# Kernel optimization log

Hardware: AMD Instinct MI355X
Metric: run time of the kernel (lower is better)

## Reference

```python
import jax, jax.numpy as jnp
import numpy as np

HIDDEN = 1024
HEADS = 16
HEAD_DIM = HIDDEN // HEADS
ROPE_BASE = 10000.0


def rope_cos_sin(seq_len, head_dim, dtype=jnp.float32):
    inv_freq = 1.0 / (ROPE_BASE ** (jnp.arange(0, head_dim, 2, dtype=jnp.float32) / head_dim))
    t = jnp.arange(seq_len, dtype=jnp.float32)
    freqs = jnp.einsum('i,j->ij', t, inv_freq)          # [L, head_dim/2]
    emb = jnp.concatenate([freqs, freqs], axis=-1)       # [L, head_dim]
    return emb.astype(dtype), jnp.cos(emb).astype(dtype), jnp.sin(emb).astype(dtype)


def rotate_half(x):
    half = x.shape[-1] // 2
    return jnp.concatenate([-x[..., half:], x[..., :half]], axis=-1)


def setup_inputs() -> dict:
    key = jax.random.key(0)
    kx, kq, kk, kv, ko = jax.random.split(key, 5)
    B, L = 4, 2048
    scale = 1.0 / np.sqrt(HIDDEN)
    x = jax.random.normal(kx, (B, L, HIDDEN), dtype=jnp.float32)
    Wq = jax.random.normal(kq, (HIDDEN, HIDDEN), dtype=jnp.float32) * scale
    Wk = jax.random.normal(kk, (HIDDEN, HIDDEN), dtype=jnp.float32) * scale
    Wv = jax.random.normal(kv, (HIDDEN, HIDDEN), dtype=jnp.float32) * scale
    Wo = jax.random.normal(ko, (HIDDEN, HIDDEN), dtype=jnp.float32) * scale
    return {"x": x, "Wq": Wq, "Wk": Wk, "Wv": Wv, "Wo": Wo}


def reference(x, Wq, Wk, Wv, Wo):
    B, L, D = x.shape
    H, Hd = HEADS, HEAD_DIM
    # projections (nn.Linear: y = x @ W.T; weights here stored already as [out,in])
    q = (x @ Wq.T).reshape(B, L, H, Hd).transpose(0, 2, 1, 3)  # [B,H,L,Hd]
    k = (x @ Wk.T).reshape(B, L, H, Hd).transpose(0, 2, 1, 3)
    v = (x @ Wv.T).reshape(B, L, H, Hd).transpose(0, 2, 1, 3)
    _, cos, sin = rope_cos_sin(L, Hd, x.dtype)                  # [L, Hd]
    cos = cos[None, None, :, :]
    sin = sin[None, None, :, :]
    q = q * cos + rotate_half(q) * sin
    k = k * cos + rotate_half(k) * sin
    scores = jnp.einsum('bhqd,bhkd->bhqk', q, k) / np.sqrt(Hd)  # [B,H,L,L]
    attn = jax.nn.softmax(scores, axis=-1)
    out = jnp.einsum('bhqk,bhkd->bhqd', attn, v)                # [B,H,L,Hd]
    out = out.transpose(0, 2, 1, 3).reshape(B, L, D)
    return out @ Wo.T
```

## Files before the change

kernel.cpp:

```cpp
#include <hip/hip_runtime.h>
#include <math.h>

#define BB 4
#define LL 2048
#define DD 1024
#define HH 16
#define HD 64
#define BL (BB*LL)

typedef __attribute__((ext_vector_type(8))) short bf16x8;
typedef __attribute__((ext_vector_type(4))) short bf16x4;
typedef __attribute__((ext_vector_type(4))) float f32x4;

__device__ inline short f2bf(float f) {
    union { float f; unsigned u; } v; v.f = f;
    unsigned r = v.u + 0x7fffu + ((v.u >> 16) & 1u);
    return (short)(r >> 16);
}

__device__ inline unsigned pk_bf16(float a, float b) {
    union { float f; unsigned u; } x, y; x.f = a; y.f = b;
    return (x.u >> 16) | (y.u & 0xffff0000u);
}

__device__ inline float exp2x(float x) {
#if __has_builtin(__builtin_amdgcn_exp2f)
    return __builtin_amdgcn_exp2f(x);
#else
    return exp2f(x);
#endif
}

__device__ inline f32x4 mfma16x16x16_bf16(bf16x4 a, bf16x4 b, f32x4 c) {
#if __has_builtin(__builtin_amdgcn_mfma_f32_16x16x16bf16_1k)
    return __builtin_amdgcn_mfma_f32_16x16x16bf16_1k(a, b, c, 0, 0, 0);
#elif __has_builtin(__builtin_amdgcn_mfma_f32_16x16x16_bf16)
    return __builtin_amdgcn_mfma_f32_16x16x16_bf16(a, b, c, 0, 0, 0);
#else
    f32x4 d;
    asm volatile("v_mfma_f32_16x16x16_bf16 %0, %1, %2, %3"
                 : "=v"(d) : "v"(a), "v"(b), "v"(c));
    return d;
#endif
}

__device__ inline void gload_lds16(const void* g, void* l) {
    __builtin_amdgcn_global_load_lds(
        (const __attribute__((address_space(1))) unsigned int*)g,
        (__attribute__((address_space(3))) unsigned int*)l, 16, 0, 0);
}

__global__ __launch_bounds__(256) void cast_kernel(
    const float* __restrict__ in, short* __restrict__ out, int n)
{
    int i = (blockIdx.x * 256 + threadIdx.x) * 8;
    float4 a = *(const float4*)(in + i);
    float4 b = *(const float4*)(in + i + 4);
    bf16x8 o;
    o[0]=f2bf(a.x); o[1]=f2bf(a.y); o[2]=f2bf(a.z); o[3]=f2bf(a.w);
    o[4]=f2bf(b.x); o[5]=f2bf(b.y); o[6]=f2bf(b.z); o[7]=f2bf(b.w);
    *(bf16x8*)(out + i) = o;
}

__global__ __launch_bounds__(256) void cast4_kernel(
    const float* __restrict__ w0, const float* __restrict__ w1,
    const float* __restrict__ w2, const float* __restrict__ w3,
    short* __restrict__ out)
{
    const int nw_blocks = (DD*DD) / 2048;
    int sel = blockIdx.x / nw_blocks;
    int blk = blockIdx.x % nw_blocks;
    const float* in = (sel == 0) ? w0 : (sel == 1) ? w1 : (sel == 2) ? w2 : w3;
    int i = (blk * 256 + threadIdx.x) * 8;
    float4 a = *(const float4*)(in + i);
    float4 b = *(const float4*)(in + i + 4);
    bf16x8 o;
    o[0]=f2bf(a.x); o[1]=f2bf(a.y); o[2]=f2bf(a.z); o[3]=f2bf(a.w);
    o[4]=f2bf(b.x); o[5]=f2bf(b.y); o[6]=f2bf(b.z); o[7]=f2bf(b.w);
    *(bf16x8*)(out + (size_t)sel * DD * DD + i) = o;
}

__global__ __launch_bounds__(256) void rope_tab_kernel(float2* __restrict__ tab)
{
    int idx = blockIdx.x * 256 + threadIdx.x;
    int lq = idx >> 5, f = idx & 31;
    float inv = __expf((float)f * (-9.210340371976184f / 32.0f));
    float s, c;
    sincosf((float)lq * inv, &s, &c);
    tab[idx] = make_float2(c, s);
}

__device__ inline void gemm_bt_128(const short* __restrict__ A,
                                   const short* __restrict__ B,
                                   short* Ash, short* Bsh,
                                   int i0, int n0, f32x4 (&acc)[4][4])
{
    const int t  = threadIdx.x;
    const int w  = t >> 6;
    const int l  = t & 63;
    const int g  = (t >> 4) & 3;
    const int ln = t & 15;
    const int rh = (w >> 1) * 64;
    const int ch = (w & 1) * 64;
    const int srow = w * 8 + (l >> 3);
    const int skol = (l & 7) * 8;

    for (int k0 = 0; k0 < DD; k0 += 64) {
        __syncthreads();
        const short* ga = A + (size_t)(i0 + srow) * DD + k0 + skol;
        const short* gb = B + (size_t)(n0 + srow) * DD + k0 + skol;
        short* la = Ash + w * 512;
        short* lb = Bsh + w * 512;
        #pragma unroll
        for (int j = 0; j < 4; ++j) {
            gload_lds16(ga + j * 32 * DD, la + j * 2048);
            gload_lds16(gb + j * 32 * DD, lb + j * 2048);
        }
        __syncthreads();

        #pragma unroll
        for (int kk = 0; kk < 2; ++kk) {
            bf16x8 af[4], bfr[4];
            #pragma unroll
            for (int mi = 0; mi < 4; ++mi)
                af[mi] = *(const bf16x8*)(Ash + (rh + mi*16 + ln)*64 + kk*32 + 8*g);
            #pragma unroll
            for (int nj = 0; nj < 4; ++nj)
                bfr[nj] = *(const bf16x8*)(Bsh + (ch + nj*16 + ln)*64 + kk*32 + 8*g);
            #pragma unroll
            for (int mi = 0; mi < 4; ++mi)
                #pragma unroll
                for (int nj = 0; nj < 4; ++nj)
                    acc[mi][nj] = __builtin_amdgcn_mfma_f32_16x16x32_bf16(
                        af[mi], bfr[nj], acc[mi][nj], 0, 0, 0);
        }
    }
}

__global__ __launch_bounds__(256) void qkv_mfma_kernel(
    const short* __restrict__ xb, const short* __restrict__ Wqb,
    const short* __restrict__ Wkb, const short* __restrict__ Wvb,
    const float2* __restrict__ rope_tab,
    short* __restrict__ Qo, short* __restrict__ Ko, short* __restrict__ Vo)
{
    __shared__ short Ash[128*64];
    __shared__ short Bsh[128*64];

    const int gid = blockIdx.x;
    const int r8  = gid & 7;
    const int u   = gid >> 3;
    const int i_idx = r8 * 8 + (u & 7);
    const int nz  = u >> 3;
    const int n_idx = nz & 7;
    const int z   = nz >> 3;

    const short* Wm = (z == 0) ? Wqb : ((z == 1) ? Wkb : Wvb);
    const int i0 = i_idx * 128;
    const int n0 = n_idx * 128;

    f32x4 acc[4][4];
    #pragma unroll
    for (int mi = 0; mi < 4; ++mi)
        #pragma unroll
        for (int nj = 0; nj < 4; ++nj) acc[mi][nj] = (f32x4){0.f,0.f,0.f,0.f};

    gemm_bt_128(xb, Wm, Ash, Bsh, i0, n0, acc);

    const int t  = threadIdx.x;
    const int w  = t >> 6;
    const int g  = (t >> 4) & 3;
    const int ln = t & 15;
    const int rh = (w >> 1) * 64;

    if (z == 2) {
        short* buf = Ash;
        const int b = i0 >> 11, l0 = i0 & (LL - 1);
        const int d = t >> 2;
        const int c = t & 3;
        #pragma unroll
        for (int hp = 0; hp < 2; ++hp) {
            __syncthreads();
            if ((w & 1) == hp) {
                #pragma unroll
                for (int nj = 0; nj < 4; ++nj)
                    #pragma unroll
                    for (int mi = 0; mi < 4; ++mi)
                        #pragma unroll
                        for (int r = 0; r < 4; ++r)
                            buf[(nj*16 + ln)*136 + rh + mi*16 + 4*g + r]
                                = f2bf(acc[mi][nj][r]);
            }
            __syncthreads();
            short* dst = Vo + ((size_t)((b*HH + n_idx*2 + hp)*HD + d)) * LL + l0;
            #pragma unroll
            for (int j = 0; j < 4; ++j)
                *(bf16x8*)(dst + c*8 + j*32) =
                    *(const bf16x8*)(buf + d*136 + c*8 + j*32);
        }
    } else {
        const int h = n_idx * 2 + (w & 1);
        short* Om = (z == 0) ? Qo : Ko;
        const float sc = (z == 0) ? 0.180336880111112f : 1.0f;
        #pragma unroll
        for (int mi = 0; mi < 4; ++mi)
            #pragma unroll
            for (int r = 0; r < 4; ++r) {
                int i = i0 + rh + mi*16 + 4*g + r;
                int b = i >> 11, lq = i & (LL - 1);
                float2 cs0 = rope_tab[lq*32 + ln];
                float2 cs1 = rope_tab[lq*32 + ln + 16];
                float r0 = (acc[mi][0][r]*cs0.x - acc[mi][2][r]*cs0.y) * sc;
                float r2 = (acc[mi][2][r]*cs0.x + acc[mi][0][r]*cs0.y) * sc;
                float r1 = (acc[mi][1][r]*cs1.x - acc[mi][3][r]*cs1.y) * sc;
                float r3 = (acc[mi][3][r]*cs1.x + acc[mi][1][r]*cs1.y) * sc;
                size_t base = ((size_t)(b*HH + h) * LL + lq) * HD;
                Om[base + ln     ] = f2bf(r0);
                Om[base + ln + 16] = f2bf(r1);
                Om[base + ln + 32] = f2bf(r2);
                Om[base + ln + 48] = f2bf(r3);
            }
    }
}

__global__ __launch_bounds__(256) void attn_kernel(
    const short* __restrict__ Q, const short* __restrict__ K,
    const short* __restrict__ VT, short* __restrict__ AO)
{
    __shared__ short Ksh[64*72];
    __shared__ short VTs[64*72];

    const int t  = threadIdx.x;
    const int w  = t >> 6;
    const int l  = t & 63;
    const int g  = l >> 4;
    const int ln = l & 15;

    const int bh = blockIdx.x;
    const int q0 = blockIdx.y * 128;
    const short* Qb  = Q  + ((size_t)bh * LL + q0 + w*32) * HD;
    const short* Kb  = K  + (size_t)bh * LL * HD;
    const short* VTb = VT + (size_t)bh * HD * LL;

    bf16x8 qb[2][2];
    #pragma unroll
    for (int qi = 0; qi < 2; ++qi) {
        qb[qi][0] = *(const bf16x8*)(Qb + (size_t)(qi*16 + ln)*HD + 8*g);
        qb[qi][1] = *(const bf16x8*)(Qb + (size_t)(qi*16 + ln)*HD + 32 + 8*g);
    }

    f32x4 O[2][4];
    #pragma unroll
    for (int qi = 0; qi < 2; ++qi)
        #pragma unroll
        for (int db = 0; db < 4; ++db) O[qi][db] = (f32x4){0.f,0.f,0.f,0.f};
    float l_acc[2] = {0.f, 0.f};

    const int sr = t >> 2;
    const int sc = (t & 3) << 4;

    for (int kt = 0; kt < LL; kt += 64) {
        bf16x8 k0 = *(const bf16x8*)(Kb  + (size_t)(kt + sr)*HD + sc);
        bf16x8 k1 = *(const bf16x8*)(Kb  + (size_t)(kt + sr)*HD + sc + 8);
        bf16x8 v0 = *(const bf16x8*)(VTb + (size_t)sr*LL + kt + sc);
        bf16x8 v1 = *(const bf16x8*)(VTb + (size_t)sr*LL + kt + sc + 8);
        __syncthreads();
        *(bf16x8*)(Ksh + sr*72 + sc)     = k0;
        *(bf16x8*)(Ksh + sr*72 + sc + 8) = k1;
        *(bf16x8*)(VTs + sr*72 + sc)     = v0;
        *(bf16x8*)(VTs + sr*72 + sc + 8) = v1;
        __syncthreads();

        uint2 pf[2][4];
        #pragma unroll
        for (int kb = 0; kb < 4; ++kb) {
            bf16x8 ka0 = *(const bf16x8*)(Ksh + (kb*16 + ln)*72 + 8*g);
            bf16x8 ka1 = *(const bf16x8*)(Ksh + (kb*16 + ln)*72 + 32 + 8*g);
            #pragma unroll
            for (int qi = 0; qi < 2; ++qi) {
                f32x4 S = (f32x4){0.f,0.f,0.f,0.f};
                S = __builtin_amdgcn_mfma_f32_16x16x32_bf16(ka0, qb[qi][0], S, 0, 0, 0);
                S = __builtin_amdgcn_mfma_f32_16x16x32_bf16(ka1, qb[qi][1], S, 0, 0, 0);
                float p0 = exp2x(S[0]), p1 = exp2x(S[1]);
                float p2 = exp2x(S[2]), p3 = exp2x(S[3]);
                l_acc[qi] += (p0 + p1) + (p2 + p3);
                pf[qi][kb].x = pk_bf16(p0, p1);
                pf[qi][kb].y = pk_bf16(p2, p3);
            }
        }

        #pragma unroll
        for (int kb = 0; kb < 4; ++kb) {
            bf16x4 pa0 = __builtin_bit_cast(bf16x4, pf[0][kb]);
            bf16x4 pa1 = __builtin_bit_cast(bf16x4, pf[1][kb]);
            #pragma unroll
            for (int db = 0; db < 4; ++db) {
                bf16x4 vf = *(const bf16x4*)(VTs + (db*16 + ln)*72 + kb*16 + 4*g);
                O[0][db] = mfma16x16x16_bf16(pa0, vf, O[0][db]);
                O[1][db] = mfma16x16x16_bf16(pa1, vf, O[1][db]);
            }
        }
    }

    const int b = bh >> 4, h = bh & 15;
    #pragma unroll
    for (int qi = 0; qi < 2; ++qi) {
        float lr = l_acc[qi];
        lr += __shfl_xor(lr, 16);
        lr += __shfl_xor(lr, 32);
        #pragma unroll
        for (int r = 0; r < 4; ++r) {
            float inv = 1.0f / __shfl(lr, 4*g + r);
            int q = q0 + w*32 + qi*16 + 4*g + r;
            size_t base = ((size_t)(b*LL + q)) * DD + h*HD;
            #pragma unroll
            for (int db = 0; db < 4; ++db)
                AO[base + db*16 + ln] = f2bf(O[qi][db][r] * inv);
        }
    }
}

__global__ __launch_bounds__(256) void oproj_mfma_kernel(
    const short* __restrict__ A, const short* __restrict__ Wob,
    float* __restrict__ out)
{
    __shared__ short Ash[128*64];
    __shared__ short Bsh[128*64];

    const int gid = blockIdx.x;
    const int r8  = gid & 7;
    const int u   = gid >> 3;
    const int i_idx = r8 * 8 + (u & 7);
    const int n_idx = u >> 3;
    const int i0 = i_idx * 128;
    const int n0 = n_idx * 128;

    f32x4 acc[4][4];
    #pragma unroll
    for (int mi = 0; mi < 4; ++mi)
        #pragma unroll
        for (int nj = 0; nj < 4; ++nj) acc[mi][nj] = (f32x4){0.f,0.f,0.f,0.f};

    gemm_bt_128(A, Wob, Ash, Bsh, i0, n0, acc);

    const int t  = threadIdx.x;
    const int w  = t >> 6;
    const int g  = (t >> 4) & 3;
    const int ln = t & 15;
    const int rh = (w >> 1) * 64;
    const int ch = (w & 1) * 64;

    #pragma unroll
    for (int mi = 0; mi < 4; ++mi)
        #pragma unroll
        for (int r = 0; r < 4; ++r) {
            size_t base = (size_t)(i0 + rh + mi*16 + 4*g + r) * DD + n0 + ch;
            #pragma unroll
            for (int nj = 0; nj < 4; ++nj)
                out[base + nj*16 + ln] = acc[mi][nj][r];
        }
}

extern "C" void kernel_launch(void* const* d_in, const int* in_sizes, int n_in,
                              void* d_out, int out_size, void* d_ws, size_t ws_size,
                              hipStream_t stream) {
    const float* x  = (const float*)d_in[0];
    const float* Wq = (const float*)d_in[1];
    const float* Wk = (const float*)d_in[2];
    const float* Wv = (const float*)d_in[3];
    const float* Wo = (const float*)d_in[4];
    float* out = (float*)d_out;

    const size_t n_x = (size_t)BL * DD;
    const size_t n_w = (size_t)DD * DD;
    short* xb  = (short*)d_ws;
    short* Wqb = xb  + n_x;
    short* Wkb = Wqb + n_w;
    short* Wvb = Wkb + n_w;
    short* Wob = Wvb + n_w;
    short* Q   = Wob + n_w;
    short* K   = Q   + n_x;
    short* VTg = K   + n_x;
    short* AOb = VTg + n_x;
    float2* tab = (float2*)(AOb + n_x);

    rope_tab_kernel<<<256, 256, 0, stream>>>(tab);
    cast_kernel<<<n_x/2048, 256, 0, stream>>>(x, xb, (int)n_x);
    cast4_kernel<<<4*(n_w/2048), 256, 0, stream>>>(Wq, Wk, Wv, Wo, Wqb);

    qkv_mfma_kernel<<<1536, 256, 0, stream>>>(xb, Wqb, Wkb, Wvb, tab, Q, K, VTg);

    dim3 g2(BB*HH, LL/128);
    attn_kernel<<<g2, 256, 0, stream>>>(Q, K, VTg, AOb);

    oproj_mfma_kernel<<<512, 256, 0, stream>>>(AOb, Wob, out);
}
```

Before: 290.8 us.

## Load K fragments directly to registers and use 16x16x32 MFMA for PV

Removes the K shared-memory staging in the attention loop, so each wave loads its K MFMA fragments straight from global memory into registers. This drops LDS writes and reads for K but makes the four waves redundantly load the same K tile from global/L2. The P·V product now uses the wider 16x16x32 bf16 MFMA by packing two 16-key P fragments into one operand and concatenating two V sub-fragments, halving the MFMA count for that stage.

```diff
diff --git a/kernel.cpp b/kernel.cpp
--- a/kernel.cpp
+++ b/kernel.cpp
@@ -28,19 +28,6 @@
     return __builtin_amdgcn_exp2f(x);
 #else
     return exp2f(x);
-#endif
-}
-
-__device__ inline f32x4 mfma16x16x16_bf16(bf16x4 a, bf16x4 b, f32x4 c) {
-#if __has_builtin(__builtin_amdgcn_mfma_f32_16x16x16bf16_1k)
-    return __builtin_amdgcn_mfma_f32_16x16x16bf16_1k(a, b, c, 0, 0, 0);
-#elif __has_builtin(__builtin_amdgcn_mfma_f32_16x16x16_bf16)
-    return __builtin_amdgcn_mfma_f32_16x16x16_bf16(a, b, c, 0, 0, 0);
-#else
-    f32x4 d;
-    asm volatile("v_mfma_f32_16x16x16_bf16 %0, %1, %2, %3"
-                 : "=v"(d) : "v"(a), "v"(b), "v"(c));
-    return d;
 #endif
 }
 
@@ -226,7 +213,6 @@
     const short* __restrict__ Q, const short* __restrict__ K,
     const short* __restrict__ VT, short* __restrict__ AO)
 {
-    __shared__ short Ksh[64*72];
     __shared__ short VTs[64*72];
 
     const int t  = threadIdx.x;
@@ -259,44 +245,52 @@
     const int sc = (t & 3) << 4;
 
     for (int kt = 0; kt < LL; kt += 64) {
-        bf16x8 k0 = *(const bf16x8*)(Kb  + (size_t)(kt + sr)*HD + sc);
-        bf16x8 k1 = *(const bf16x8*)(Kb  + (size_t)(kt + sr)*HD + sc + 8);
         bf16x8 v0 = *(const bf16x8*)(VTb + (size_t)sr*LL + kt + sc);
         bf16x8 v1 = *(const bf16x8*)(VTb + (size_t)sr*LL + kt + sc + 8);
+        bf16x8 ka[4][2];
+        #pragma unroll
+        for (int kb = 0; kb < 4; ++kb) {
+            const short* kp = Kb + (size_t)(kt + kb*16 + ln) * HD + 8*g;
+            ka[kb][0] = *(const bf16x8*)(kp);
+            ka[kb][1] = *(const bf16x8*)(kp + 32);
+        }
         __syncthreads();
-        *(bf16x8*)(Ksh + sr*72 + sc)     = k0;
-        *(bf16x8*)(Ksh + sr*72 + sc + 8) = k1;
         *(bf16x8*)(VTs + sr*72 + sc)     = v0;
         *(bf16x8*)(VTs + sr*72 + sc + 8) = v1;
         __syncthreads();
 
-        uint2 pf[2][4];
+        unsigned pf[2][4][2];
         #pragma unroll
         for (int kb = 0; kb < 4; ++kb) {
-            bf16x8 ka0 = *(const bf16x8*)(Ksh + (kb*16 + ln)*72 + 8*g);
-            bf16x8 ka1 = *(const bf16x8*)(Ksh + (kb*16 + ln)*72 + 32 + 8*g);
             #pragma unroll
             for (int qi = 0; qi < 2; ++qi) {
                 f32x4 S = (f32x4){0.f,0.f,0.f,0.f};
-                S = __builtin_amdgcn_mfma_f32_16x16x32_bf16(ka0, qb[qi][0], S, 0, 0, 0);
-                S = __builtin_amdgcn_mfma_f32_16x16x32_bf16(ka1, qb[qi][1], S, 0, 0, 0);
+                S = __builtin_amdgcn_mfma_f32_16x16x32_bf16(ka[kb][0], qb[qi][0], S, 0, 0, 0);
+                S = __builtin_amdgcn_mfma_f32_16x16x32_bf16(ka[kb][1], qb[qi][1], S, 0, 0, 0);
                 float p0 = exp2x(S[0]), p1 = exp2x(S[1]);
                 float p2 = exp2x(S[2]), p3 = exp2x(S[3]);
                 l_acc[qi] += (p0 + p1) + (p2 + p3);
-                pf[qi][kb].x = pk_bf16(p0, p1);
-                pf[qi][kb].y = pk_bf16(p2, p3);
+                pf[qi][kb][0] = pk_bf16(p0, p1);
+                pf[qi][kb][1] = pk_bf16(p2, p3);
             }
         }
 
         #pragma unroll
-        for (int kb = 0; kb < 4; ++kb) {
-            bf16x4 pa0 = __builtin_bit_cast(bf16x4, pf[0][kb]);
-            bf16x4 pa1 = __builtin_bit_cast(bf16x4, pf[1][kb]);
+        for (int b = 0; b < 2; ++b) {
             #pragma unroll
             for (int db = 0; db < 4; ++db) {
-                bf16x4 vf = *(const bf16x4*)(VTs + (db*16 + ln)*72 + kb*16 + 4*g);
-                O[0][db] = mfma16x16x16_bf16(pa0, vf, O[0][db]);
-                O[1][db] = mfma16x16x16_bf16(pa1, vf, O[1][db]);
+                const short* vp = VTs + (db*16 + ln)*72 + b*32 + 4*g;
+                bf16x4 vlo = *(const bf16x4*)(vp);
+                bf16x4 vhi = *(const bf16x4*)(vp + 16);
+                bf16x8 vf = __builtin_shufflevector(vlo, vhi, 0,1,2,3,4,5,6,7);
+                #pragma unroll
+                for (int qi = 0; qi < 2; ++qi) {
+                    union { unsigned u[4]; bf16x8 v; } a;
+                    a.u[0] = pf[qi][2*b][0];   a.u[1] = pf[qi][2*b][1];
+                    a.u[2] = pf[qi][2*b+1][0]; a.u[3] = pf[qi][2*b+1][1];
+                    O[qi][db] = __builtin_amdgcn_mfma_f32_16x16x32_bf16(
+                        a.v, vf, O[qi][db], 0, 0, 0);
+                }
             }
         }
     }
```

New measurement: 337.8 us. 1.16x slower.
